# Kernel optimization log

Measured on AMD Instinct MI355X. Metric: run time of the kernel, lower is better.

Reference implementation:

```python
import jax, jax.numpy as jnp
import numpy as np

QB = 127.0  # 8-bit activation quant range
EPS = 1e-5


def _bitlinear(x, w, b):
    # BitNet b1.58-style BitLinear.
    # Activation: per-token absmax 8-bit quantization (STE).
    s = QB / jnp.clip(jnp.max(jnp.abs(x), axis=-1, keepdims=True), EPS)
    xq = jnp.clip(jnp.round(x * s), -QB - 1.0, QB) / s
    xq = x + jax.lax.stop_gradient(xq - x)
    # Weight: ternary {-1,0,1} with absmean scaling (STE).
    ws = 1.0 / jnp.clip(jnp.mean(jnp.abs(w)), EPS)
    wq = jnp.clip(jnp.round(w * ws), -1.0, 1.0) / ws
    wq = w + jax.lax.stop_gradient(wq - w)
    return jnp.einsum('bsf,of->bso', xq, wq) + b


def setup_inputs() -> dict:
    key = jax.random.key(0)
    k1, k2, k3, k4, k5, k6 = jax.random.split(key, 6)
    B, S, F = 8, 32768, 128
    evidence = jax.random.normal(k1, (B, S, F), dtype=jnp.float32)
    prior_belief = jax.random.uniform(k2, (B, S, F), dtype=jnp.float32)
    # belief_update params: Linear(2F -> F), Linear(F -> F)
    W1 = jax.random.normal(k3, (F, 2 * F), dtype=jnp.float32) * (1.0 / np.sqrt(2 * F))
    b1 = jax.random.normal(k4, (F,), dtype=jnp.float32) * 0.01
    W2 = jax.random.normal(k5, (F, F), dtype=jnp.float32) * (1.0 / np.sqrt(F))
    b2 = jax.random.normal(k6, (F,), dtype=jnp.float32) * 0.01
    return {"evidence": evidence, "prior_belief": prior_belief,
            "W1": W1, "b1": b1, "W2": W2, "b2": b2}


def reference(evidence, prior_belief, W1, b1, W2, b2):
    # update network: BitLinear -> ReLU -> BitLinear -> Sigmoid
    upd_in = jnp.concatenate([prior_belief, evidence], axis=-1)  # [B,S,2F]
    h = jax.nn.relu(_bitlinear(upd_in, W1, b1))                  # [B,S,F]
    likelihood = jax.nn.sigmoid(_bitlinear(h, W2, b2))           # [B,S,F]
    posterior_unnorm = prior_belief * likelihood
    normalizer = jnp.clip(posterior_unnorm.sum(axis=1, keepdims=True), 1e-10)
    return posterior_unnorm / normalizer
```

## Files before the change

### kernel.cpp

```cpp
#include <hip/hip_runtime.h>
#include <hip/hip_bf16.h>
#include <math.h>

typedef int   i32x4 __attribute__((ext_vector_type(4)));
typedef unsigned int u32;

#define QBF 127.0f
#define EPSF 1e-5f
#define FF 128
#define NROWS (8 * 32768)
#define NBLK 512
#define TPB 8

#define W2_OFF    32768
#define WBUF_OFF  49152
#define CS_OFF    66560
#define LDS_TOTAL 68608

#define LGKM0() asm volatile("s_waitcnt lgkmcnt(0)" ::: "memory")
#define SB()    __builtin_amdgcn_sched_barrier(0)

static __device__ __forceinline__ float bcast_lane(float v, int lane) {
    return __builtin_bit_cast(float, __builtin_amdgcn_readlane(__builtin_bit_cast(int, v), lane));
}
static __device__ __forceinline__ u32 packi8(float a, float b, float c, float d, float s) {
    int i0 = (int)rintf(a * s), i1 = (int)rintf(b * s);
    int i2 = (int)rintf(c * s), i3 = (int)rintf(d * s);
    return (u32)(i0 & 0xFF) | ((u32)(i1 & 0xFF) << 8) |
           ((u32)(i2 & 0xFF) << 16) | ((u32)i3 << 24);
}

__global__ void pstats_kernel(const float* __restrict__ W1,
                              const float* __restrict__ W2,
                              double* __restrict__ psum) {
    __shared__ double red[256];
    int b = blockIdx.x, t = threadIdx.x;
    const float4* src = (b < 32) ? (const float4*)(W1 + b * 1024)
                                 : (const float4*)(W2 + (b - 32) * 1024);
    float4 v = src[t];
    red[t] = (double)fabsf(v.x) + (double)fabsf(v.y)
           + (double)fabsf(v.z) + (double)fabsf(v.w);
    __syncthreads();
    for (int o = 128; o > 0; o >>= 1) { if (t < o) red[t] += red[t + o]; __syncthreads(); }
    if (t == 0) psum[b] = red[0];
}

__global__ void sfinal_kernel(const double* __restrict__ psum, float* __restrict__ hdr) {
    __shared__ double red[64];
    int t = threadIdx.x;
    red[t] = (t < 32) ? psum[t] : 0.0;
    __syncthreads();
    for (int o = 16; o > 0; o >>= 1) { if (t < o) red[t] += red[t + o]; __syncthreads(); }
    double s1 = red[0];
    __syncthreads();
    red[t] = (t < 16) ? psum[32 + t] : 0.0;
    __syncthreads();
    for (int o = 8; o > 0; o >>= 1) { if (t < o) red[t] += red[t + o]; __syncthreads(); }
    if (t == 0) {
        hdr[0] = 1.0f / fmaxf((float)(s1 * (1.0 / 32768.0)), EPSF);
        hdr[1] = 1.0f / fmaxf((float)(red[0] * (1.0 / 16384.0)), EPSF);
    }
}

__global__ void wquant_kernel(const float* __restrict__ W1,
                              const float* __restrict__ W2,
                              const float* __restrict__ hdr,
                              char* __restrict__ wq) {
    int g = blockIdx.x * 256 + threadIdx.x;
    float ws1 = hdr[0], ws2 = hdr[1];
    const float* src; float wsx; char* dst;
    if (g < 2048) {
        int gi = g >> 6, l = g & 63;
        int ct = gi >> 2, kb = gi & 3;
        src = W1 + (ct * 16 + (l & 15)) * 256 + kb * 64 + (l >> 4) * 16;
        wsx = ws1;
        dst = wq + gi * 1024 + l * 16;
    } else {
        int g2 = g - 2048;
        int gi = g2 >> 6, l = g2 & 63;
        int ct = gi >> 1, kb = gi & 1;
        src = W2 + (ct * 16 + (l & 15)) * 128 + kb * 64 + (l >> 4) * 16;
        wsx = ws2;
        dst = wq + 32768 + gi * 1024 + l * 16;
    }
    u32 o[4];
    #pragma unroll
    for (int q = 0; q < 4; ++q) {
        float4 v = *(const float4*)(src + q * 4);
        float q0 = fminf(fmaxf(rintf(v.x * wsx), -1.f), 1.f);
        float q1 = fminf(fmaxf(rintf(v.y * wsx), -1.f), 1.f);
        float q2 = fminf(fmaxf(rintf(v.z * wsx), -1.f), 1.f);
        float q3 = fminf(fmaxf(rintf(v.w * wsx), -1.f), 1.f);
        o[q] = packi8(q0, q1, q2, q3, 1.0f);
    }
    *(uint4*)dst = make_uint4(o[0], o[1], o[2], o[3]);
}

__global__ __launch_bounds__(256, 2) void fused_kernel(
    const float* __restrict__ evid, const float* __restrict__ prior,
    const float* __restrict__ bias1, const float* __restrict__ bias2,
    const char* __restrict__ wq, const float* __restrict__ hdr,
    float* __restrict__ out, float* __restrict__ partials)
{
    __shared__ __align__(16) char smem[LDS_TOTAL];
    const int tid = threadIdx.x;
    const int w = tid >> 6, l = tid & 63;
    const int lr = l & 15, lg = l >> 4;
    const int lc = l & 31, half = l >> 5;
    char* wbuf = smem + WBUF_OFF + w * 4352;
    float* colsum = (float*)(smem + CS_OFF);
    const float ws1 = hdr[0], ws2 = hdr[1];

    {
        const uint4* g = (const uint4*)wq;
        #pragma unroll
        for (int i = 0; i < 12; ++i) {
            uint4 v = g[i * 256 + tid];
            *(uint4*)(smem + (size_t)(i * 256 + tid) * 16) = v;
        }
    }
    float4 xr[16];
    {
        const float* srcp = half ? evid : prior;
        int R0 = blockIdx.x * 512 + w * 16;
        #pragma unroll
        for (int r = 0; r < 16; ++r)
            xr[r] = *(const float4*)(srcp + (size_t)(R0 + r) * FF + lc * 4);
    }
    __syncthreads();

    float4 cs[2];
    cs[0] = make_float4(0.f, 0.f, 0.f, 0.f);
    cs[1] = make_float4(0.f, 0.f, 0.f, 0.f);

    for (int t = 0; t < TPB; ++t) {
        const int R0c = blockIdx.x * 512 + t * 64 + w * 16;

        #pragma unroll
        for (int r = 0; r < 16; ++r) {
            float4 v = xr[r];
            float m = fmaxf(fmaxf(fabsf(v.x), fabsf(v.y)),
                            fmaxf(fabsf(v.z), fabsf(v.w)));
            *(float*)(wbuf + r * 272 + l * 4) = m;
        }
        LGKM0(); SB();
        float mm;
        {
            const char* p = wbuf + lr * 272 + lg * 64;
            float4 a = *(const float4*)(p);
            float4 b = *(const float4*)(p + 16);
            float4 c = *(const float4*)(p + 32);
            float4 d = *(const float4*)(p + 48);
            float m0 = fmaxf(fmaxf(a.x, a.y), fmaxf(a.z, a.w));
            float m1 = fmaxf(fmaxf(b.x, b.y), fmaxf(b.z, b.w));
            float m2 = fmaxf(fmaxf(c.x, c.y), fmaxf(c.z, c.w));
            float m3 = fmaxf(fmaxf(d.x, d.y), fmaxf(d.z, d.w));
            mm = fmaxf(fmaxf(m0, m1), fmaxf(m2, m3));
        }
        mm = fmaxf(mm, __shfl_xor(mm, 16, 64));
        mm = fmaxf(mm, __shfl_xor(mm, 32, 64));
        const float sA = QBF / fmaxf(mm, EPSF);
        const float rinv1 = 1.0f / (sA * ws1);

        #pragma unroll
        for (int r = 0; r < 16; ++r) {
            float s_r = bcast_lane(sA, r);
            float4 v = xr[r];
            *(u32*)(wbuf + r * 272 + l * 4) = packi8(v.x, v.y, v.z, v.w, s_r);
        }

        if (t + 1 < TPB) {
            const float* srcp = half ? evid : prior;
            int R0n = blockIdx.x * 512 + (t + 1) * 64 + w * 16;
            #pragma unroll
            for (int r = 0; r < 8; ++r)
                xr[r] = *(const float4*)(srcp + (size_t)(R0n + r) * FF + lc * 4);
        }
        LGKM0(); SB();

        i32x4 acc1[8] = {};
        #pragma unroll
        for (int kb = 0; kb < 4; ++kb) {
            i32x4 xb = *(const i32x4*)(wbuf + lr * 272 + kb * 64 + lg * 16);
            #pragma unroll
            for (int ct = 0; ct < 8; ++ct) {
                i32x4 wa = *(const i32x4*)(smem + (ct * 4 + kb) * 1024 + l * 16);
                acc1[ct] = __builtin_amdgcn_mfma_i32_16x16x64_i8(wa, xb, acc1[ct], 0, 0, 0);
            }
        }

        float h[8][4];
        float hmax = 0.f;
        #pragma unroll
        for (int ct = 0; ct < 8; ++ct) {
            float4 b4 = *(const float4*)(bias1 + ct * 16 + lg * 4);
            h[ct][0] = fmaxf((float)acc1[ct][0] * rinv1 + b4.x, 0.f);
            h[ct][1] = fmaxf((float)acc1[ct][1] * rinv1 + b4.y, 0.f);
            h[ct][2] = fmaxf((float)acc1[ct][2] * rinv1 + b4.z, 0.f);
            h[ct][3] = fmaxf((float)acc1[ct][3] * rinv1 + b4.w, 0.f);
            hmax = fmaxf(hmax, fmaxf(fmaxf(h[ct][0], h[ct][1]),
                                     fmaxf(h[ct][2], h[ct][3])));
        }
        hmax = fmaxf(hmax, __shfl_xor(hmax, 16, 64));
        hmax = fmaxf(hmax, __shfl_xor(hmax, 32, 64));
        const float s2 = QBF / fmaxf(hmax, EPSF);
        const float rinv2 = 1.0f / (s2 * ws2);

        #pragma unroll
        for (int ct = 0; ct < 8; ++ct)
            *(u32*)(wbuf + lr * 272 + ct * 16 + lg * 4) =
                packi8(h[ct][0], h[ct][1], h[ct][2], h[ct][3], s2);

        if (t + 1 < TPB) {
            const float* srcp = half ? evid : prior;
            int R0n = blockIdx.x * 512 + (t + 1) * 64 + w * 16;
            #pragma unroll
            for (int r = 8; r < 16; ++r)
                xr[r] = *(const float4*)(srcp + (size_t)(R0n + r) * FF + lc * 4);
        }
        float4 pvr[8];
        #pragma unroll
        for (int p = 0; p < 2; ++p) {
            #pragma unroll
            for (int i = 0; i < 4; ++i) {
                int rloc = 4 * i + (l >> 4);
                pvr[p * 4 + i] = *(const float4*)(prior +
                    (size_t)(R0c + rloc) * FF + p * 64 + (l & 15) * 4);
            }
        }
        LGKM0(); SB();

        i32x4 acc2[8] = {};
        #pragma unroll
        for (int kb = 0; kb < 2; ++kb) {
            i32x4 hb = *(const i32x4*)(wbuf + lr * 272 + kb * 64 + lg * 16);
            #pragma unroll
            for (int ct = 0; ct < 8; ++ct) {
                i32x4 wa = *(const i32x4*)(smem + W2_OFF + (ct * 2 + kb) * 1024 + l * 16);
                acc2[ct] = __builtin_amdgcn_mfma_i32_16x16x64_i8(wa, hb, acc2[ct], 0, 0, 0);
            }
        }

        #pragma unroll
        for (int p = 0; p < 2; ++p) {
            #pragma unroll
            for (int c = 0; c < 4; ++c) {
                const int ct = 4 * p + c;
                float4 b4 = *(const float4*)(bias2 + ct * 16 + lg * 4);
                float4 lik;
                float y0 = (float)acc2[ct][0] * rinv2 + b4.x;
                float y1 = (float)acc2[ct][1] * rinv2 + b4.y;
                float y2 = (float)acc2[ct][2] * rinv2 + b4.z;
                float y3 = (float)acc2[ct][3] * rinv2 + b4.w;
                lik.x = __builtin_amdgcn_rcpf(1.0f + __expf(-y0));
                lik.y = __builtin_amdgcn_rcpf(1.0f + __expf(-y1));
                lik.z = __builtin_amdgcn_rcpf(1.0f + __expf(-y2));
                lik.w = __builtin_amdgcn_rcpf(1.0f + __expf(-y3));
                *(float4*)(wbuf + lr * 272 + c * 64 + lg * 16) = lik;
            }
            LGKM0(); SB();
            #pragma unroll
            for (int i = 0; i < 4; ++i) {
                int rloc = 4 * i + (l >> 4);
                float4 lk = *(const float4*)(wbuf + rloc * 272 + (l & 15) * 16);
                float4 pv = pvr[p * 4 + i];
                float4 un;
                un.x = pv.x * lk.x; un.y = pv.y * lk.y;
                un.z = pv.z * lk.z; un.w = pv.w * lk.w;
                *(float4*)(out + (size_t)(R0c + rloc) * FF + p * 64 + (l & 15) * 4) = un;
                cs[p].x += un.x; cs[p].y += un.y;
                cs[p].z += un.z; cs[p].w += un.w;
            }
            LGKM0(); SB();
        }
    }

    #pragma unroll
    for (int p = 0; p < 2; ++p) {
        cs[p].x += __shfl_xor(cs[p].x, 16, 64);
        cs[p].y += __shfl_xor(cs[p].y, 16, 64);
        cs[p].z += __shfl_xor(cs[p].z, 16, 64);
        cs[p].w += __shfl_xor(cs[p].w, 16, 64);
        cs[p].x += __shfl_xor(cs[p].x, 32, 64);
        cs[p].y += __shfl_xor(cs[p].y, 32, 64);
        cs[p].z += __shfl_xor(cs[p].z, 32, 64);
        cs[p].w += __shfl_xor(cs[p].w, 32, 64);
    }
    if (l < 16) {
        *(float4*)(colsum + w * 128 + l * 4) = cs[0];
        *(float4*)(colsum + w * 128 + 64 + l * 4) = cs[1];
    }
    __syncthreads();
    if (tid < FF) {
        float p = colsum[tid] + colsum[128 + tid]
                + colsum[256 + tid] + colsum[384 + tid];
        partials[(size_t)blockIdx.x * FF + tid] = p;
    }
}

__global__ void norm_kernel(const float* __restrict__ partials, float* __restrict__ norm) {
    __shared__ float red[2][128];
    int b = blockIdx.x;
    int f = threadIdx.x & 127, tg = threadIdx.x >> 7;
    float s = 0.f;
    for (int t = tg * 32; t < tg * 32 + 32; ++t)
        s += partials[((size_t)b * 64 + t) * FF + f];
    red[tg][f] = s; __syncthreads();
    if (tg == 0)
        norm[b * FF + f] = fmaxf(red[0][f] + red[1][f], 1e-10f);
}

__global__ void div_kernel(float* __restrict__ out, const float* __restrict__ norm) {
    size_t i4 = (size_t)blockIdx.x * blockDim.x + threadIdx.x;
    const size_t total4 = (size_t)NROWS * FF / 4;
    for (; i4 < total4; i4 += (size_t)gridDim.x * blockDim.x) {
        size_t i = i4 * 4;
        float4 v = *(float4*)(out + i);
        int b = (int)(i >> 22);
        int f = (int)(i & 127);
        float4 nv = *(const float4*)(norm + b * FF + f);
        v.x /= nv.x; v.y /= nv.y; v.z /= nv.z; v.w /= nv.w;
        *(float4*)(out + i) = v;
    }
}

extern "C" void kernel_launch(void* const* d_in, const int* in_sizes, int n_in,
                              void* d_out, int out_size, void* d_ws, size_t ws_size,
                              hipStream_t stream) {
    const float* evid  = (const float*)d_in[0];
    const float* prior = (const float*)d_in[1];
    const float* W1    = (const float*)d_in[2];
    const float* b1    = (const float*)d_in[3];
    const float* W2    = (const float*)d_in[4];
    const float* b2    = (const float*)d_in[5];
    float* out = (float*)d_out;

    char* ws = (char*)d_ws;
    float*  hdr      = (float*)ws;
    double* psum     = (double*)(ws + 256);
    char*   wq       = ws + 1024;
    float*  partials = (float*)(ws + 65536);
    float*  norm     = (float*)(ws + 65536 + 262144);

    pstats_kernel<<<48, 256, 0, stream>>>(W1, W2, psum);
    sfinal_kernel<<<1, 64, 0, stream>>>(psum, hdr);
    wquant_kernel<<<12, 256, 0, stream>>>(W1, W2, hdr, wq);
    fused_kernel<<<NBLK, 256, 0, stream>>>(evid, prior, b1, b2, wq, hdr, out, partials);
    norm_kernel<<<8, 256, 0, stream>>>(partials, norm);
    div_kernel<<<2048, 256, 0, stream>>>(out, norm);
}
```

Baseline: 158.4 us.

## Raise fused kernel occupancy to three blocks per CU with uneven tile split

The grid grows from 512 to 768 blocks, each handling 5 or 6 tiles of 64 rows within one batch, so the grid covers the CUs more evenly. To fit three blocks per CU, the W2 weights are no longer staged in LDS; the second MFMA reads them directly from global memory, and launch bounds are raised to 3. Prior-belief loads are moved after the second GEMM and loaded per half to cut register pressure. The risk is extra global or L2 traffic for the W2 fragments on every tile, and tighter register limits that could cause spills.

After: 180.2 us. +13.8%, slower.

```diff
diff --git a/kernel.cpp b/kernel.cpp
--- a/kernel.cpp
+++ b/kernel.cpp
@@ -9,13 +9,12 @@
 #define EPSF 1e-5f
 #define FF 128
 #define NROWS (8 * 32768)
-#define NBLK 512
-#define TPB 8
-
-#define W2_OFF    32768
-#define WBUF_OFF  49152
-#define CS_OFF    66560
-#define LDS_TOTAL 68608
+#define NBLK 768
+#define BPB 96
+
+#define WBUF_OFF  32768
+#define CS_OFF    (32768 + 4 * 4352)
+#define LDS_TOTAL (CS_OFF + 2048)
 
 #define LGKM0() asm volatile("s_waitcnt lgkmcnt(0)" ::: "memory")
 #define SB()    __builtin_amdgcn_sched_barrier(0)
@@ -96,7 +95,7 @@
     *(uint4*)dst = make_uint4(o[0], o[1], o[2], o[3]);
 }
 
-__global__ __launch_bounds__(256, 2) void fused_kernel(
+__global__ __launch_bounds__(256, 3) void fused_kernel(
     const float* __restrict__ evid, const float* __restrict__ prior,
     const float* __restrict__ bias1, const float* __restrict__ bias2,
     const char* __restrict__ wq, const float* __restrict__ hdr,
@@ -110,19 +109,26 @@
     char* wbuf = smem + WBUF_OFF + w * 4352;
     float* colsum = (float*)(smem + CS_OFF);
     const float ws1 = hdr[0], ws2 = hdr[1];
+    const char* wq2g = wq + 32768;
+
+    const int batch = blockIdx.x / BPB;
+    const int b96   = blockIdx.x % BPB;
+    const int nt    = (b96 < 32) ? 6 : 5;
+    const int t0    = (b96 < 32) ? b96 * 6 : 192 + (b96 - 32) * 5;
+    const int rowbase_b = batch * 32768;
+    const float* srcp = half ? evid : prior;
 
     {
         const uint4* g = (const uint4*)wq;
         #pragma unroll
-        for (int i = 0; i < 12; ++i) {
+        for (int i = 0; i < 8; ++i) {
             uint4 v = g[i * 256 + tid];
             *(uint4*)(smem + (size_t)(i * 256 + tid) * 16) = v;
         }
     }
     float4 xr[16];
     {
-        const float* srcp = half ? evid : prior;
-        int R0 = blockIdx.x * 512 + w * 16;
+        int R0 = rowbase_b + t0 * 64 + w * 16;
         #pragma unroll
         for (int r = 0; r < 16; ++r)
             xr[r] = *(const float4*)(srcp + (size_t)(R0 + r) * FF + lc * 4);
@@ -133,8 +139,9 @@
     cs[0] = make_float4(0.f, 0.f, 0.f, 0.f);
     cs[1] = make_float4(0.f, 0.f, 0.f, 0.f);
 
-    for (int t = 0; t < TPB; ++t) {
-        const int R0c = blockIdx.x * 512 + t * 64 + w * 16;
+    for (int ti = 0; ti < nt; ++ti) {
+        const int t = t0 + ti;
+        const int R0c = rowbase_b + t * 64 + w * 16;
 
         #pragma unroll
         for (int r = 0; r < 16; ++r) {
@@ -169,9 +176,8 @@
             *(u32*)(wbuf + r * 272 + l * 4) = packi8(v.x, v.y, v.z, v.w, s_r);
         }
 
-        if (t + 1 < TPB) {
-            const float* srcp = half ? evid : prior;
-            int R0n = blockIdx.x * 512 + (t + 1) * 64 + w * 16;
+        if (ti + 1 < nt) {
+            int R0n = rowbase_b + (t + 1) * 64 + w * 16;
             #pragma unroll
             for (int r = 0; r < 8; ++r)
                 xr[r] = *(const float4*)(srcp + (size_t)(R0n + r) * FF + lc * 4);
@@ -211,38 +217,34 @@
             *(u32*)(wbuf + lr * 272 + ct * 16 + lg * 4) =
                 packi8(h[ct][0], h[ct][1], h[ct][2], h[ct][3], s2);
 
-        if (t + 1 < TPB) {
-            const float* srcp = half ? evid : prior;
-            int R0n = blockIdx.x * 512 + (t + 1) * 64 + w * 16;
+        if (ti + 1 < nt) {
+            int R0n = rowbase_b + (t + 1) * 64 + w * 16;
             #pragma unroll
             for (int r = 8; r < 16; ++r)
                 xr[r] = *(const float4*)(srcp + (size_t)(R0n + r) * FF + lc * 4);
         }
-        float4 pvr[8];
+        LGKM0(); SB();
+
+        i32x4 acc2[8] = {};
+        #pragma unroll
+        for (int kb = 0; kb < 2; ++kb) {
+            i32x4 hb = *(const i32x4*)(wbuf + lr * 272 + kb * 64 + lg * 16);
+            #pragma unroll
+            for (int ct = 0; ct < 8; ++ct) {
+                i32x4 wa = *(const i32x4*)(wq2g + (ct * 2 + kb) * 1024 + l * 16);
+                acc2[ct] = __builtin_amdgcn_mfma_i32_16x16x64_i8(wa, hb, acc2[ct], 0, 0, 0);
+            }
+        }
+
         #pragma unroll
         for (int p = 0; p < 2; ++p) {
+            float4 pvp[4];
             #pragma unroll
             for (int i = 0; i < 4; ++i) {
                 int rloc = 4 * i + (l >> 4);
-                pvr[p * 4 + i] = *(const float4*)(prior +
+                pvp[i] = *(const float4*)(prior +
                     (size_t)(R0c + rloc) * FF + p * 64 + (l & 15) * 4);
             }
-        }
-        LGKM0(); SB();
-
-        i32x4 acc2[8] = {};
-        #pragma unroll
-        for (int kb = 0; kb < 2; ++kb) {
-            i32x4 hb = *(const i32x4*)(wbuf + lr * 272 + kb * 64 + lg * 16);
-            #pragma unroll
-            for (int ct = 0; ct < 8; ++ct) {
-                i32x4 wa = *(const i32x4*)(smem + W2_OFF + (ct * 2 + kb) * 1024 + l * 16);
-                acc2[ct] = __builtin_amdgcn_mfma_i32_16x16x64_i8(wa, hb, acc2[ct], 0, 0, 0);
-            }
-        }
-
-        #pragma unroll
-        for (int p = 0; p < 2; ++p) {
             #pragma unroll
             for (int c = 0; c < 4; ++c) {
                 const int ct = 4 * p + c;
@@ -263,7 +265,7 @@
             for (int i = 0; i < 4; ++i) {
                 int rloc = 4 * i + (l >> 4);
                 float4 lk = *(const float4*)(wbuf + rloc * 272 + (l & 15) * 16);
-                float4 pv = pvr[p * 4 + i];
+                float4 pv = pvp[i];
                 float4 un;
                 un.x = pv.x * lk.x; un.y = pv.y * lk.y;
                 un.z = pv.z * lk.z; un.w = pv.w * lk.w;
@@ -303,8 +305,8 @@
     int b = blockIdx.x;
     int f = threadIdx.x & 127, tg = threadIdx.x >> 7;
     float s = 0.f;
-    for (int t = tg * 32; t < tg * 32 + 32; ++t)
-        s += partials[((size_t)b * 64 + t) * FF + f];
+    for (int k = tg * 48; k < tg * 48 + 48; ++k)
+        s += partials[((size_t)b * BPB + k) * FF + f];
     red[tg][f] = s; __syncthreads();
     if (tg == 0)
         norm[b * FF + f] = fmaxf(red[0][f] + red[1][f], 1e-10f);
@@ -340,7 +342,7 @@
     double* psum     = (double*)(ws + 256);
     char*   wq       = ws + 1024;
     float*  partials = (float*)(ws + 65536);
-    float*  norm     = (float*)(ws + 65536 + 262144);
+    float*  norm     = (float*)(ws + 65536 + 393216);
 
     pstats_kernel<<<48, 256, 0, stream>>>(W1, W2, psum);
     sfinal_kernel<<<1, 64, 0, stream>>>(psum, hdr);
```
